# Performance work log

Hardware: AMD Instinct MI355X
Metric: run time of the kernel (lower is better)

The kernel has to match this reference:

```python
import jax, jax.numpy as jnp
import numpy as np

MODEL_DIM = 1024
NUM_HEADS = 16
HEAD_DIM = MODEL_DIM // NUM_HEADS


def _rope(t):
    # t: [B, S, H, hd] -- ESM-style rotary (rotate_half on halves, freqs tiled)
    B, S, H, hd = t.shape
    inv_freq = 1.0 / (10000.0 ** (jnp.arange(0, hd, 2, dtype=jnp.float32) / hd))  # [hd/2]
    freqs = jnp.arange(S, dtype=jnp.float32)[:, None] * inv_freq[None, :]          # [S, hd/2]
    emb = jnp.concatenate([freqs, freqs], axis=-1)                                 # [S, hd]
    cos = jnp.cos(emb)[None, :, None, :].astype(t.dtype)
    sin = jnp.sin(emb)[None, :, None, :].astype(t.dtype)
    t1, t2 = jnp.split(t, 2, axis=-1)
    rot = jnp.concatenate([-t2, t1], axis=-1)
    return t * cos + rot * sin


def setup_inputs() -> dict:
    key = jax.random.key(0)
    ks = jax.random.split(key, 5)
    D = MODEL_DIM
    s = 1.0 / np.sqrt(D)
    return {
        "x": jax.random.normal(ks[0], (2, 2048, D), dtype=jnp.float32),
        "in_proj_w": jax.random.normal(ks[1], (3 * D, D), dtype=jnp.float32) * s,
        "in_proj_b": jax.random.normal(ks[2], (3 * D,), dtype=jnp.float32) * 0.02,
        "out_proj_w": jax.random.normal(ks[3], (D, D), dtype=jnp.float32) * s,
        "out_proj_b": jax.random.normal(ks[4], (D,), dtype=jnp.float32) * 0.02,
    }


def reference(x, in_proj_w, in_proj_b, out_proj_w, out_proj_b):
    B, S, D = x.shape
    H, hd = NUM_HEADS, HEAD_DIM
    # --- manual _in_proj using MHA's packed in_proj params ---
    combined = jnp.einsum('bsd,ed->bse', x, in_proj_w) + in_proj_b  # [B,S,3D]
    q0, k0, v0 = jnp.split(combined, 3, axis=-1)
    # --- rotary on q/k per head ---
    q1 = _rope(q0.reshape(B, S, H, hd)).reshape(B, S, D)
    k1 = _rope(k0.reshape(B, S, H, hd)).reshape(B, S, D)
    # --- nn.MultiheadAttention re-projects q/k/v with the SAME in_proj ---
    Wq, Wk, Wv = in_proj_w[:D], in_proj_w[D:2 * D], in_proj_w[2 * D:]
    bq, bk, bv = in_proj_b[:D], in_proj_b[D:2 * D], in_proj_b[2 * D:]
    q = (jnp.einsum('bsd,ed->bse', q1, Wq) + bq).reshape(B, S, H, hd)
    k = (jnp.einsum('bsd,ed->bse', k1, Wk) + bk).reshape(B, S, H, hd)
    v = (jnp.einsum('bsd,ed->bse', v0, Wv) + bv).reshape(B, S, H, hd)
    # --- scaled dot-product attention ---
    scale = 1.0 / np.sqrt(hd)
    scores = jnp.einsum('bqhd,bkhd->bhqk', q, k) * scale
    attn = jax.nn.softmax(scores, axis=-1)
    ctx = jnp.einsum('bhqk,bkhd->bqhd', attn, v).reshape(B, S, D)
    return jnp.einsum('bsd,ed->bse', ctx, out_proj_w) + out_proj_b
```

## Files before the change

kernel.cpp:

```cpp
#include <hip/hip_runtime.h>
#include <math.h>

#define D_MODEL   1024
#define N_HEADS   16
#define H_DIM     64
#define SEQ       2048
#define BATCH     2
#define ROWS      (BATCH * SEQ)
#define THREE_D   (3 * D_MODEL)

#define QK_SCALE  (0.125f * 1.44269504088896340736f)

typedef __attribute__((ext_vector_type(8))) short short8v;
typedef __attribute__((ext_vector_type(4))) float f32x4;
typedef __attribute__((ext_vector_type(4))) unsigned int uint4v;
typedef __attribute__((ext_vector_type(2))) unsigned int uint2v;

union Frag { uint4v u; short8v s; };

__device__ __forceinline__ void async_copy16(const void* g, void* l)
{
    __builtin_amdgcn_global_load_lds(
        (const __attribute__((address_space(1))) void*)g,
        (__attribute__((address_space(3))) void*)l,
        16, 0, 0);
}

__device__ __forceinline__ int swz8(int row, int oct)
{
    return oct ^ ((row ^ (row >> 2)) & 7);
}

__device__ __forceinline__ void split2x8(const float* v, uint4v& U1, uint4v& U2)
{
    unsigned b1[8], b2[8];
#pragma unroll
    for (int j = 0; j < 8; ++j) {
        const unsigned u = __float_as_uint(v[j]);
        b1[j] = u;
        const float r = v[j] - __uint_as_float(u & 0xFFFF0000u);
        b2[j] = __float_as_uint(r);
    }
    U1 = (uint4v){ (b1[0]>>16)|(b1[1]&0xFFFF0000u), (b1[2]>>16)|(b1[3]&0xFFFF0000u),
                   (b1[4]>>16)|(b1[5]&0xFFFF0000u), (b1[6]>>16)|(b1[7]&0xFFFF0000u) };
    U2 = (uint4v){ (b2[0]>>16)|(b2[1]&0xFFFF0000u), (b2[2]>>16)|(b2[3]&0xFFFF0000u),
                   (b2[4]>>16)|(b2[5]&0xFFFF0000u), (b2[6]>>16)|(b2[7]&0xFFFF0000u) };
}

__device__ __forceinline__ void pack_store(unsigned short* rowp, int col, float val)
{
    unsigned short* d = rowp + ((col >> 5) << 6) + (col & 31);
    const unsigned u = __float_as_uint(val);
    d[0]  = (unsigned short)(u >> 16);
    const float r = val - __uint_as_float(u & 0xFFFF0000u);
    d[32] = (unsigned short)(__float_as_uint(r) >> 16);
}

__global__ __launch_bounds__(256)
void split_pack(const float* __restrict__ in, unsigned short* __restrict__ out)
{
    const size_t e0 = ((size_t)blockIdx.x * 256 + threadIdx.x) * 8;
    const float4 a0 = *reinterpret_cast<const float4*>(in + e0);
    const float4 a1 = *reinterpret_cast<const float4*>(in + e0 + 4);
    float v[8] = { a0.x, a0.y, a0.z, a0.w, a1.x, a1.y, a1.z, a1.w };
    uint4v U1, U2;
    split2x8(v, U1, U2);
    unsigned short* d = out + ((e0 >> 5) << 6) + (e0 & 31);
    *reinterpret_cast<uint4v*>(d)      = U1;
    *reinterpret_cast<uint4v*>(d + 32) = U2;
}

__global__ void rope_table(float* __restrict__ tab)
{
    const int idx = blockIdx.x * 256 + threadIdx.x;
    const int s = idx >> 5;
    const int i = idx & 31;
    const double inv = pow(10000.0, -(double)(2 * i) / 64.0);
    const double f = (double)s * inv;
    tab[idx * 2 + 0] = (float)cos(f);
    tab[idx * 2 + 1] = (float)sin(f);
}

__global__ __launch_bounds__(256, 2)
void gemm_p(const unsigned short* __restrict__ Ap, int ldA2,
            const unsigned short* __restrict__ Bp, int ldB2,
            const float* __restrict__ bias,
            float* __restrict__ C, int ldc, int K,
            int nbx, size_t segA, size_t segB, int segBias, size_t segC)
{
    __shared__ __align__(16) unsigned short As[2][128 * 64];
    __shared__ __align__(16) unsigned short Bs[2][128 * 64];

    const int seg = blockIdx.x / nbx;
    const int bxs = blockIdx.x - seg * nbx;
    const int bm  = blockIdx.y * 128;
    const int bn  = bxs * 128;
    Ap   += (size_t)seg * segA;
    Bp   += (size_t)seg * segB;
    bias += seg * segBias;
    C    += (size_t)seg * segC;

    const int t    = threadIdx.x;
    const int wid  = t >> 6;
    const int lane = t & 63;
    const int wr   = wid >> 1;
    const int wc   = wid & 1;
    const int cl   = lane & 15;
    const int kq   = lane >> 4;
    const int lrow = lane >> 3;
    const int gs   = lane & 7;

    auto stage = [&](int buf, int k0) {
        const int gl = gs ^ lrow;
#pragma unroll
        for (int q = 0; q < 4; ++q) {
            const int r0  = (wid * 4 + q) * 8;
            const int row = r0 + lrow;
            async_copy16(Ap + (size_t)(bm + row) * ldA2 + (k0 << 1) + (gl << 3),
                         &As[buf][r0 * 64]);
            async_copy16(Bp + (size_t)(bn + row) * ldB2 + (k0 << 1) + (gl << 3),
                         &Bs[buf][r0 * 64]);
        }
    };

    f32x4 acc[4][4];
#pragma unroll
    for (int m = 0; m < 4; ++m)
#pragma unroll
        for (int n = 0; n < 4; ++n) acc[m][n] = (f32x4)(0.f);

    const int NT = K >> 5;
    stage(0, 0);

    for (int it = 0; it < NT; ++it) {
        __syncthreads();
        if (it + 1 < NT)
            stage((it + 1) & 1, (it + 1) << 5);

        const unsigned short* as = As[it & 1];
        const unsigned short* bs = Bs[it & 1];

        short8v A1[4], A2[4], B1[4], B2[4];
#pragma unroll
        for (int m = 0; m < 4; ++m) {
            const int r = wr * 64 + m * 16 + cl;
            const unsigned short* ar = as + r * 64;
            A1[m] = *reinterpret_cast<const short8v*>(ar + (( kq      ^ (r & 7)) << 3));
            A2[m] = *reinterpret_cast<const short8v*>(ar + (((kq + 4) ^ (r & 7)) << 3));
        }
#pragma unroll
        for (int n = 0; n < 4; ++n) {
            const int r = wc * 64 + n * 16 + cl;
            const unsigned short* br = bs + r * 64;
            B1[n] = *reinterpret_cast<const short8v*>(br + (( kq      ^ (r & 7)) << 3));
            B2[n] = *reinterpret_cast<const short8v*>(br + (((kq + 4) ^ (r & 7)) << 3));
        }

#pragma unroll
        for (int m = 0; m < 4; ++m)
#pragma unroll
            for (int n = 0; n < 4; ++n) {
                f32x4 c = acc[m][n];
                c = __builtin_amdgcn_mfma_f32_16x16x32_bf16(A1[m], B1[n], c, 0, 0, 0);
                c = __builtin_amdgcn_mfma_f32_16x16x32_bf16(A2[m], B1[n], c, 0, 0, 0);
                c = __builtin_amdgcn_mfma_f32_16x16x32_bf16(A1[m], B2[n], c, 0, 0, 0);
                acc[m][n] = c;
            }
    }

    const int rw = lane >> 4;
#pragma unroll
    for (int n = 0; n < 4; ++n) {
        const int col = bn + wc * 64 + n * 16 + cl;
        const float bv = bias[col];
#pragma unroll
        for (int m = 0; m < 4; ++m) {
            const size_t rbase = (size_t)(bm + wr * 64 + m * 16 + rw * 4);
#pragma unroll
            for (int i = 0; i < 4; ++i)
                C[(rbase + i) * ldc + col] = acc[m][n][i] + bv;
        }
    }
}

__global__ __launch_bounds__(256, 2)
void gemm_p_rope(const unsigned short* __restrict__ Ap, int ldA2,
                 const unsigned short* __restrict__ Bp, int ldB2,
                 const float* __restrict__ bias,
                 const float* __restrict__ tab,
                 unsigned short* __restrict__ out, int K)
{
    __shared__ __align__(16) unsigned short As[2][128 * 64];
    __shared__ __align__(16) unsigned short Bs[2][128 * 64];

    const int bm  = blockIdx.y * 128;
    const int bn  = blockIdx.x * 128;

    const int t    = threadIdx.x;
    const int wid  = t >> 6;
    const int lane = t & 63;
    const int wr   = wid >> 1;
    const int wc   = wid & 1;
    const int cl   = lane & 15;
    const int kq   = lane >> 4;
    const int lrow = lane >> 3;
    const int gs   = lane & 7;

    auto stage = [&](int buf, int k0) {
        const int gl = gs ^ lrow;
#pragma unroll
        for (int q = 0; q < 4; ++q) {
            const int r0  = (wid * 4 + q) * 8;
            const int row = r0 + lrow;
            async_copy16(Ap + (size_t)(bm + row) * ldA2 + (k0 << 1) + (gl << 3),
                         &As[buf][r0 * 64]);
            async_copy16(Bp + (size_t)(bn + row) * ldB2 + (k0 << 1) + (gl << 3),
                         &Bs[buf][r0 * 64]);
        }
    };

    f32x4 acc[4][4];
#pragma unroll
    for (int m = 0; m < 4; ++m)
#pragma unroll
        for (int n = 0; n < 4; ++n) acc[m][n] = (f32x4)(0.f);

    const int NT = K >> 5;
    stage(0, 0);

    for (int it = 0; it < NT; ++it) {
        __syncthreads();
        if (it + 1 < NT)
            stage((it + 1) & 1, (it + 1) << 5);

        const unsigned short* as = As[it & 1];
        const unsigned short* bs = Bs[it & 1];

        short8v A1[4], A2[4], B1[4], B2[4];
#pragma unroll
        for (int m = 0; m < 4; ++m) {
            const int r = wr * 64 + m * 16 + cl;
            const unsigned short* ar = as + r * 64;
            A1[m] = *reinterpret_cast<const short8v*>(ar + (( kq      ^ (r & 7)) << 3));
            A2[m] = *reinterpret_cast<const short8v*>(ar + (((kq + 4) ^ (r & 7)) << 3));
        }
#pragma unroll
        for (int n = 0; n < 4; ++n) {
            const int r = wc * 64 + n * 16 + cl;
            const unsigned short* br = bs + r * 64;
            B1[n] = *reinterpret_cast<const short8v*>(br + (( kq      ^ (r & 7)) << 3));
            B2[n] = *reinterpret_cast<const short8v*>(br + (((kq + 4) ^ (r & 7)) << 3));
        }

#pragma unroll
        for (int m = 0; m < 4; ++m)
#pragma unroll
            for (int n = 0; n < 4; ++n) {
                f32x4 c = acc[m][n];
                c = __builtin_amdgcn_mfma_f32_16x16x32_bf16(A1[m], B1[n], c, 0, 0, 0);
                c = __builtin_amdgcn_mfma_f32_16x16x32_bf16(A2[m], B1[n], c, 0, 0, 0);
                c = __builtin_amdgcn_mfma_f32_16x16x32_bf16(A1[m], B2[n], c, 0, 0, 0);
                acc[m][n] = c;
            }
    }

    const int rw = lane >> 4;
    const bool doRope = (bn < 2 * D_MODEL);
#pragma unroll
    for (int n = 0; n < 2; ++n) {
        const int colA = bn + wc * 64 + n * 16 + cl;
        const int colB = colA + 32;
        const float bvA = bias[colA];
        const float bvB = bias[colB];
        const int d = n * 16 + cl;
#pragma unroll
        for (int m = 0; m < 4; ++m) {
            const size_t rbase = (size_t)(bm + wr * 64 + m * 16 + rw * 4);
#pragma unroll
            for (int i = 0; i < 4; ++i) {
                const size_t row = rbase + i;
                const float t1 = acc[m][n][i]     + bvA;
                const float t2 = acc[m][n + 2][i] + bvB;
                float r1 = t1, r2 = t2;
                if (doRope) {
                    const int s = (int)(row & (SEQ - 1));
                    const float c  = tab[(s * 32 + d) * 2 + 0];
                    const float sn = tab[(s * 32 + d) * 2 + 1];
                    r1 = t1 * c - t2 * sn;
                    r2 = t2 * c + t1 * sn;
                }
                unsigned short* op = out + row * (size_t)(THREE_D * 2);
                pack_store(op, colA, r1);
                pack_store(op, colB, r2);
            }
        }
    }
}

__global__ __launch_bounds__(512)
void attn_mfma(const float* __restrict__ Qg, const float* __restrict__ Kg,
               const float* __restrict__ Vg, unsigned short* __restrict__ pctx)
{
    __shared__ __align__(16) short Ks1[64 * 64];
    __shared__ __align__(16) short Ks2[64 * 64];
    __shared__ __align__(16) short Vt1[64 * 64];
    __shared__ __align__(16) short Vt2[64 * 64];
    __shared__ __align__(16) short Ps[8 * 16 * 64];

    const int fid = blockIdx.y * gridDim.x + blockIdx.x;
    const int bh  = (fid & 7) * 4 + ((fid >> 3) & 3);
    const int q0  = (fid >> 5) * 128;
    const int b   = bh >> 4;
    const int h   = bh & 15;
    const size_t rowBase = (size_t)b * SEQ;
    const int hOff = h * H_DIM;

    const int t    = threadIdx.x;
    const int w    = t >> 6;
    const int lane = t & 63;
    const int cl   = lane & 15;
    const int g    = lane >> 4;

    const int krow = t >> 2;
    const int dob  = (t & 3) * 2;
    const int t2   = t - 256;
    const int vkq  = t2 >> 4;
    const int vdq  = t2 & 15;

    Frag qf[2][2];
#pragma unroll
    for (int c = 0; c < 2; ++c) {
        const float* qp = Qg + (rowBase + q0 + w * 16 + cl) * D_MODEL
                          + hOff + c * 32 + g * 8;
        const float4 f0 = *reinterpret_cast<const float4*>(qp);
        const float4 f1 = *reinterpret_cast<const float4*>(qp + 4);
        float v[8] = { f0.x * QK_SCALE, f0.y * QK_SCALE, f0.z * QK_SCALE, f0.w * QK_SCALE,
                       f1.x * QK_SCALE, f1.y * QK_SCALE, f1.z * QK_SCALE, f1.w * QK_SCALE };
        split2x8(v, qf[c][0].u, qf[c][1].u);
    }

    f32x4 acc[4];
#pragma unroll
    for (int s = 0; s < 4; ++s) acc[s] = (f32x4)(0.f);
    float m = -1e30f;
    float l = 0.f;

    short* pb1 = Ps + (w * 16 + cl) * 64;

    float4 sr0, sr1, sr2, sr3;

    auto load_tile = [&](int k0) {
        if (w < 4) {
            const float* kp = Kg + (rowBase + k0 + krow) * D_MODEL + hOff + dob * 8;
            sr0 = reinterpret_cast<const float4*>(kp)[0];
            sr1 = reinterpret_cast<const float4*>(kp)[1];
            sr2 = reinterpret_cast<const float4*>(kp)[2];
            sr3 = reinterpret_cast<const float4*>(kp)[3];
        } else {
            const float* vp = Vg + (rowBase + k0 + vkq * 4) * D_MODEL + hOff + vdq * 4;
            sr0 = *reinterpret_cast<const float4*>(vp);
            sr1 = *reinterpret_cast<const float4*>(vp + D_MODEL);
            sr2 = *reinterpret_cast<const float4*>(vp + 2 * D_MODEL);
            sr3 = *reinterpret_cast<const float4*>(vp + 3 * D_MODEL);
        }
    };

    auto write_tile = [&]() {
        if (w < 4) {
            float v[16];
            *reinterpret_cast<float4*>(&v[0])  = sr0;
            *reinterpret_cast<float4*>(&v[4])  = sr1;
            *reinterpret_cast<float4*>(&v[8])  = sr2;
            *reinterpret_cast<float4*>(&v[12]) = sr3;
            uint4v a1, a2, b1, b2;
            split2x8(v,     a1, a2);
            split2x8(v + 8, b1, b2);
            short* kb1 = Ks1 + krow * 64;
            short* kb2 = Ks2 + krow * 64;
            *reinterpret_cast<uint4v*>(kb1 + swz8(krow, dob    ) * 8) = a1;
            *reinterpret_cast<uint4v*>(kb1 + swz8(krow, dob + 1) * 8) = b1;
            *reinterpret_cast<uint4v*>(kb2 + swz8(krow, dob    ) * 8) = a2;
            *reinterpret_cast<uint4v*>(kb2 + swz8(krow, dob + 1) * 8) = b2;
        } else {
            float va[4][4];
            *reinterpret_cast<float4*>(va[0]) = sr0;
            *reinterpret_cast<float4*>(va[1]) = sr1;
            *reinterpret_cast<float4*>(va[2]) = sr2;
            *reinterpret_cast<float4*>(va[3]) = sr3;
            const int lo = vkq >> 1;
            const int hf = (vkq & 1) * 4;
#pragma unroll
            for (int rr = 0; rr < 4; ++rr) {
                const int row = 4 * vdq + rr;
                unsigned ub[4], rb[4];
#pragma unroll
                for (int r = 0; r < 4; ++r) {
                    const float x = va[r][rr];
                    const unsigned u = __float_as_uint(x);
                    ub[r] = u;
                    rb[r] = __float_as_uint(x - __uint_as_float(u & 0xFFFF0000u));
                }
                uint2v w1, w2;
                w1.x = (ub[0] >> 16) | (ub[1] & 0xFFFF0000u);
                w1.y = (ub[2] >> 16) | (ub[3] & 0xFFFF0000u);
                w2.x = (rb[0] >> 16) | (rb[1] & 0xFFFF0000u);
                w2.y = (rb[2] >> 16) | (rb[3] & 0xFFFF0000u);
                const int o = row * 64 + swz8(row, lo) * 8 + hf;
                *reinterpret_cast<uint2v*>(&Vt1[o]) = w1;
                *reinterpret_cast<uint2v*>(&Vt2[o]) = w2;
            }
        }
    };

    const int NT = SEQ / 64;

    load_tile(0);
    write_tile();

    for (int it = 0; it < NT; ++it) {
        __syncthreads();
        if (it + 1 < NT)
            load_tile((it + 1) * 64);

        f32x4 sacc[4];
#pragma unroll
        for (int ks = 0; ks < 4; ++ks) sacc[ks] = (f32x4)(0.f);

#pragma unroll
        for (int ks = 0; ks < 4; ++ks)
#pragma unroll
            for (int c = 0; c < 2; ++c) {
                const int row = ks * 16 + cl;
                const int po  = row * 64 + swz8(row, 4 * c + g) * 8;
                Frag ka1, ka2;
                ka1.s = *reinterpret_cast<const short8v*>(&Ks1[po]);
                ka2.s = *reinterpret_cast<const short8v*>(&Ks2[po]);
                f32x4 s = sacc[ks];
                s = __builtin_amdgcn_mfma_f32_16x16x32_bf16(ka1.s, qf[c][0].s, s, 0, 0, 0);
                s = __builtin_amdgcn_mfma_f32_16x16x32_bf16(ka2.s, qf[c][0].s, s, 0, 0, 0);
                s = __builtin_amdgcn_mfma_f32_16x16x32_bf16(ka1.s, qf[c][1].s, s, 0, 0, 0);
                sacc[ks] = s;
            }

        float tm = -1e30f;
#pragma unroll
        for (int ks = 0; ks < 4; ++ks)
#pragma unroll
            for (int i = 0; i < 4; ++i) tm = fmaxf(tm, sacc[ks][i]);
        tm = fmaxf(tm, __shfl_xor(tm, 16));
        tm = fmaxf(tm, __shfl_xor(tm, 32));

        const float mn = fmaxf(m, tm);
        const float sc = __builtin_amdgcn_exp2f(m - mn);
        m = mn;

        float rs = 0.f;
        uint2v P1[4];
#pragma unroll
        for (int ks = 0; ks < 4; ++ks) {
            float p[4];
            unsigned ub[4];
#pragma unroll
            for (int i = 0; i < 4; ++i) {
                p[i] = __builtin_amdgcn_exp2f(sacc[ks][i] - mn);
                rs += p[i];
                ub[i] = __float_as_uint(p[i]);
            }
            P1[ks] = (uint2v){ (ub[0] >> 16) | (ub[1] & 0xFFFF0000u),
                               (ub[2] >> 16) | (ub[3] & 0xFFFF0000u) };
        }
        rs += __shfl_xor(rs, 16);
        rs += __shfl_xor(rs, 32);
        l = l * sc + rs;

        float scv[4];
#pragma unroll
        for (int i = 0; i < 4; ++i) scv[i] = __shfl(sc, 4 * g + i);
#pragma unroll
        for (int s = 0; s < 4; ++s)
#pragma unroll
            for (int i = 0; i < 4; ++i) acc[s][i] *= scv[i];

#pragma unroll
        for (int ks = 0; ks < 4; ++ks) {
            const int off = swz8(cl, 2 * ks + (g >> 1)) * 8 + (g & 1) * 4;
            *reinterpret_cast<uint2v*>(pb1 + off) = P1[ks];
        }

#pragma unroll
        for (int c = 0; c < 2; ++c) {
            const int po = swz8(cl, 4 * c + g) * 8;
            Frag pa1;
            pa1.s = *reinterpret_cast<const short8v*>(pb1 + po);
#pragma unroll
            for (int s = 0; s < 4; ++s) {
                const int row = s * 16 + cl;
                const int vo  = row * 64 + swz8(row, 4 * c + g) * 8;
                Frag vb1, vb2;
                vb1.s = *reinterpret_cast<const short8v*>(&Vt1[vo]);
                vb2.s = *reinterpret_cast<const short8v*>(&Vt2[vo]);
                f32x4 a = acc[s];
                a = __builtin_amdgcn_mfma_f32_16x16x32_bf16(pa1.s, vb1.s, a, 0, 0, 0);
                a = __builtin_amdgcn_mfma_f32_16x16x32_bf16(pa1.s, vb2.s, a, 0, 0, 0);
                acc[s] = a;
            }
        }

        __syncthreads();
        if (it + 1 < NT)
            write_tile();
    }

    const float inv = 1.f / l;
    float iv[4];
#pragma unroll
    for (int i = 0; i < 4; ++i) iv[i] = __shfl(inv, 4 * g + i);
#pragma unroll
    for (int s = 0; s < 4; ++s)
#pragma unroll
        for (int i = 0; i < 4; ++i) {
            const float val = acc[s][i] * iv[i];
            const size_t grow = rowBase + q0 + w * 16 + 4 * g + i;
            const int gc = hOff + s * 16 + cl;
            pack_store(pctx + grow * (size_t)(D_MODEL * 2), gc, val);
        }
}

extern "C" void kernel_launch(void* const* d_in, const int* in_sizes, int n_in,
                              void* d_out, int out_size, void* d_ws, size_t ws_size,
                              hipStream_t stream)
{
    const float* x    = (const float*)d_in[0];
    const float* Win  = (const float*)d_in[1];
    const float* bin  = (const float*)d_in[2];
    const float* Wout = (const float*)d_in[3];
    const float* bout = (const float*)d_in[4];
    float* out = (float*)d_out;

    float* R1 = (float*)d_ws;
    float* R2 = R1 + (size_t)ROWS * THREE_D;
    unsigned short* pW  = (unsigned short*)(R2 + (size_t)ROWS * THREE_D);
    unsigned short* pWo = pW + (size_t)THREE_D * D_MODEL * 2;
    float* tab = (float*)(pWo + (size_t)D_MODEL * D_MODEL * 2);

    unsigned short* px    = (unsigned short*)R1;
    float*          qkv   = R1;
    unsigned short* pcomb = (unsigned short*)R2;
    unsigned short* pctx  = (unsigned short*)R2;

    float* qbuf = qkv;
    float* kbuf = qkv + (size_t)ROWS * D_MODEL;
    float* vbuf = kbuf + (size_t)ROWS * D_MODEL;

    const dim3 blk(256);

    rope_table<<<dim3(SEQ * 32 / 256), blk, 0, stream>>>(tab);

    split_pack<<<dim3(ROWS * D_MODEL / 8 / 256), blk, 0, stream>>>(x, px);
    split_pack<<<dim3(THREE_D * D_MODEL / 8 / 256), blk, 0, stream>>>(Win, pW);
    split_pack<<<dim3(D_MODEL * D_MODEL / 8 / 256), blk, 0, stream>>>(Wout, pWo);

    gemm_p_rope<<<dim3(24, 32), blk, 0, stream>>>(
        px, D_MODEL * 2, pW, D_MODEL * 2, bin, tab, pcomb, D_MODEL);

    gemm_p<<<dim3(24, 32), blk, 0, stream>>>(
        pcomb, THREE_D * 2, pW, D_MODEL * 2, bin, qkv, D_MODEL, D_MODEL,
        8, (size_t)(D_MODEL * 2), (size_t)D_MODEL * D_MODEL * 2, D_MODEL,
        (size_t)ROWS * D_MODEL);

    attn_mfma<<<dim3(SEQ / 128, BATCH * N_HEADS), dim3(512), 0, stream>>>(
        qbuf, kbuf, vbuf, pctx);

    gemm_p<<<dim3(8, 32), blk, 0, stream>>>(
        pctx, D_MODEL * 2, pWo, D_MODEL * 2, bout, out, D_MODEL, D_MODEL,
        8, (size_t)0, (size_t)0, 0, (size_t)0);
}
```

Before: 368.0 us.

## Double-buffer attention K/V tiles, shuffle P in registers, remap GEMM blocks per XCD

```diff
diff --git a/kernel.cpp b/kernel.cpp
--- a/kernel.cpp
+++ b/kernel.cpp
@@ -29,6 +29,14 @@
 __device__ __forceinline__ int swz8(int row, int oct)
 {
     return oct ^ ((row ^ (row >> 2)) & 7);
+}
+
+__device__ __forceinline__ uint2v shfl_u2(uint2v v, int src)
+{
+    uint2v r;
+    r.x = (unsigned)__shfl((int)v.x, src);
+    r.y = (unsigned)__shfl((int)v.y, src);
+    return r;
 }
 
 __device__ __forceinline__ void split2x8(const float* v, uint4v& U1, uint4v& U2)
@@ -91,9 +99,16 @@
     __shared__ __align__(16) unsigned short As[2][128 * 64];
     __shared__ __align__(16) unsigned short Bs[2][128 * 64];
 
-    const int seg = blockIdx.x / nbx;
-    const int bxs = blockIdx.x - seg * nbx;
-    const int bm  = blockIdx.y * 128;
+    const int fid  = blockIdx.y * gridDim.x + blockIdx.x;
+    const int bxpx = gridDim.x >> 3;
+    const int xcd  = fid & 7;
+    const int idx  = fid >> 3;
+    const int bxx  = xcd * bxpx + idx % bxpx;
+    const int by   = idx / bxpx;
+
+    const int seg = bxx / nbx;
+    const int bxs = bxx - seg * nbx;
+    const int bm  = by * 128;
     const int bn  = bxs * 128;
     Ap   += (size_t)seg * segA;
     Bp   += (size_t)seg * segB;
@@ -193,8 +208,15 @@
     __shared__ __align__(16) unsigned short As[2][128 * 64];
     __shared__ __align__(16) unsigned short Bs[2][128 * 64];
 
-    const int bm  = blockIdx.y * 128;
-    const int bn  = blockIdx.x * 128;
+    const int fid  = blockIdx.y * gridDim.x + blockIdx.x;
+    const int bxpx = gridDim.x >> 3;
+    const int xcd  = fid & 7;
+    const int idx  = fid >> 3;
+    const int bxx  = xcd * bxpx + idx % bxpx;
+    const int by   = idx / bxpx;
+
+    const int bm  = by * 128;
+    const int bn  = bxx * 128;
 
     const int t    = threadIdx.x;
     const int wid  = t >> 6;
@@ -301,11 +323,10 @@
 void attn_mfma(const float* __restrict__ Qg, const float* __restrict__ Kg,
                const float* __restrict__ Vg, unsigned short* __restrict__ pctx)
 {
-    __shared__ __align__(16) short Ks1[64 * 64];
-    __shared__ __align__(16) short Ks2[64 * 64];
-    __shared__ __align__(16) short Vt1[64 * 64];
-    __shared__ __align__(16) short Vt2[64 * 64];
-    __shared__ __align__(16) short Ps[8 * 16 * 64];
+    __shared__ __align__(16) short Ks1[2][64 * 64];
+    __shared__ __align__(16) short Ks2[2][64 * 64];
+    __shared__ __align__(16) short Vt1[2][64 * 64];
+    __shared__ __align__(16) short Vt2[2][64 * 64];
 
     const int fid = blockIdx.y * gridDim.x + blockIdx.x;
     const int bh  = (fid & 7) * 4 + ((fid >> 3) & 3);
@@ -320,6 +341,9 @@
     const int lane = t & 63;
     const int cl   = lane & 15;
     const int g    = lane >> 4;
+    const int g2   = g >> 1;
+    const int srcA = cl + 32 * (g & 1);
+    const int srcB = srcA + 16;
 
     const int krow = t >> 2;
     const int dob  = (t & 3) * 2;
@@ -344,8 +368,6 @@
     for (int s = 0; s < 4; ++s) acc[s] = (f32x4)(0.f);
     float m = -1e30f;
     float l = 0.f;
-
-    short* pb1 = Ps + (w * 16 + cl) * 64;
 
     float4 sr0, sr1, sr2, sr3;
 
@@ -365,7 +387,7 @@
         }
     };
 
-    auto write_tile = [&]() {
+    auto write_tile = [&](int buf) {
         if (w < 4) {
             float v[16];
             *reinterpret_cast<float4*>(&v[0])  = sr0;
@@ -375,8 +397,8 @@
             uint4v a1, a2, b1, b2;
             split2x8(v,     a1, a2);
             split2x8(v + 8, b1, b2);
-            short* kb1 = Ks1 + krow * 64;
-            short* kb2 = Ks2 + krow * 64;
+            short* kb1 = Ks1[buf] + krow * 64;
+            short* kb2 = Ks2[buf] + krow * 64;
             *reinterpret_cast<uint4v*>(kb1 + swz8(krow, dob    ) * 8) = a1;
             *reinterpret_cast<uint4v*>(kb1 + swz8(krow, dob + 1) * 8) = b1;
             *reinterpret_cast<uint4v*>(kb2 + swz8(krow, dob    ) * 8) = a2;
@@ -406,8 +428,8 @@
                 w2.x = (rb[0] >> 16) | (rb[1] & 0xFFFF0000u);
                 w2.y = (rb[2] >> 16) | (rb[3] & 0xFFFF0000u);
                 const int o = row * 64 + swz8(row, lo) * 8 + hf;
-                *reinterpret_cast<uint2v*>(&Vt1[o]) = w1;
-                *reinterpret_cast<uint2v*>(&Vt2[o]) = w2;
+                *reinterpret_cast<uint2v*>(&Vt1[buf][o]) = w1;
+                *reinterpret_cast<uint2v*>(&Vt2[buf][o]) = w2;
             }
         }
     };
@@ -415,10 +437,11 @@
     const int NT = SEQ / 64;
 
     load_tile(0);
-    write_tile();
+    write_tile(0);
 
     for (int it = 0; it < NT; ++it) {
         __syncthreads();
+        const int bf = it & 1;
         if (it + 1 < NT)
             load_tile((it + 1) * 64);
 
@@ -433,8 +456,8 @@
                 const int row = ks * 16 + cl;
                 const int po  = row * 64 + swz8(row, 4 * c + g) * 8;
                 Frag ka1, ka2;
-                ka1.s = *reinterpret_cast<const short8v*>(&Ks1[po]);
-                ka2.s = *reinterpret_cast<const short8v*>(&Ks2[po]);
+                ka1.s = *reinterpret_cast<const short8v*>(&Ks1[bf][po]);
+                ka2.s = *reinterpret_cast<const short8v*>(&Ks2[bf][po]);
                 f32x4 s = sacc[ks];
                 s = __builtin_amdgcn_mfma_f32_16x16x32_bf16(ka1.s, qf[c][0].s, s, 0, 0, 0);
                 s = __builtin_amdgcn_mfma_f32_16x16x32_bf16(ka2.s, qf[c][0].s, s, 0, 0, 0);
@@ -482,33 +505,31 @@
             for (int i = 0; i < 4; ++i) acc[s][i] *= scv[i];
 
 #pragma unroll
-        for (int ks = 0; ks < 4; ++ks) {
-            const int off = swz8(cl, 2 * ks + (g >> 1)) * 8 + (g & 1) * 4;
-            *reinterpret_cast<uint2v*>(pb1 + off) = P1[ks];
-        }
-
-#pragma unroll
         for (int c = 0; c < 2; ++c) {
-            const int po = swz8(cl, 4 * c + g) * 8;
-            Frag pa1;
-            pa1.s = *reinterpret_cast<const short8v*>(pb1 + po);
+            uint2v a0 = shfl_u2(P1[2 * c],     srcA);
+            uint2v a1 = shfl_u2(P1[2 * c + 1], srcA);
+            uint2v b0 = shfl_u2(P1[2 * c],     srcB);
+            uint2v b1 = shfl_u2(P1[2 * c + 1], srcB);
+            uint2v lo = g2 ? a1 : a0;
+            uint2v hi = g2 ? b1 : b0;
+            Frag pa;
+            pa.u = (uint4v){ lo.x, lo.y, hi.x, hi.y };
 #pragma unroll
             for (int s = 0; s < 4; ++s) {
                 const int row = s * 16 + cl;
                 const int vo  = row * 64 + swz8(row, 4 * c + g) * 8;
                 Frag vb1, vb2;
-                vb1.s = *reinterpret_cast<const short8v*>(&Vt1[vo]);
-                vb2.s = *reinterpret_cast<const short8v*>(&Vt2[vo]);
+                vb1.s = *reinterpret_cast<const short8v*>(&Vt1[bf][vo]);
+                vb2.s = *reinterpret_cast<const short8v*>(&Vt2[bf][vo]);
                 f32x4 a = acc[s];
-                a = __builtin_amdgcn_mfma_f32_16x16x32_bf16(pa1.s, vb1.s, a, 0, 0, 0);
-                a = __builtin_amdgcn_mfma_f32_16x16x32_bf16(pa1.s, vb2.s, a, 0, 0, 0);
+                a = __builtin_amdgcn_mfma_f32_16x16x32_bf16(pa.s, vb1.s, a, 0, 0, 0);
+                a = __builtin_amdgcn_mfma_f32_16x16x32_bf16(pa.s, vb2.s, a, 0, 0, 0);
                 acc[s] = a;
             }
         }
 
-        __syncthreads();
         if (it + 1 < NT)
-            write_tile();
+            write_tile(bf ^ 1);
     }
 
     const float inv = 1.f / l;
```

Measured after the change: 346.7 us. -5.8%, faster.
